# Kernel optimization log

Measured on AMD Instinct MI355X. Metric: run time of the kernel, lower is better.

Reference implementation:

```python
import jax, jax.numpy as jnp
import numpy as np

B, S, D, H = 2, 1024, 1024, 16
DH = D // H
EPS = 1e-5

def _ln(x, g, b):
    m = jnp.mean(x, axis=-1, keepdims=True)
    v = jnp.mean((x - m) ** 2, axis=-1, keepdims=True)
    return (x - m) / jnp.sqrt(v + EPS) * g + b

def setup_inputs() -> dict:
    key = jax.random.key(0)
    ks = jax.random.split(key, 5)
    scale = 1.0 / np.sqrt(D)
    return {
        "id": jax.random.normal(ks[0], (B, S, D), dtype=jnp.float32),
        "Wq": jax.random.uniform(ks[1], (D, D), jnp.float32, -scale, scale),
        "Wk": jax.random.uniform(ks[2], (D, D), jnp.float32, -scale, scale),
        "Wv": jax.random.uniform(ks[3], (D, D), jnp.float32, -scale, scale),
        "g0": jnp.ones((D,), jnp.float32), "b0": jnp.zeros((D,), jnp.float32),
        "g1": jnp.ones((D,), jnp.float32), "b1": jnp.zeros((D,), jnp.float32),
        "g2": jnp.ones((D,), jnp.float32), "b2": jnp.zeros((D,), jnp.float32),
    }

def reference(id, Wq, Wk, Wv, g0, b0, g1, b1, g2, b2):
    residual = id
    id_ln = _ln(id, g0, b0)
    # torch Linear: x @ W.T ; split heads along last dim, cat along batch
    q = (id_ln @ Wq.T).reshape(B, S, H, DH)
    k = (id_ln @ Wk.T).reshape(B, S, H, DH)
    v = (id_ln @ Wv.T).reshape(B, S, H, DH)
    scores = jnp.einsum('bqhd,bkhd->bhqk', q, k) / np.sqrt(DH)
    A = jax.nn.softmax(scores, axis=-1)                      # [B,H,S,S]
    O = jnp.einsum('bhqk,bkhd->bqhd', A, v).reshape(B, S, D)  # merge heads
    left = _ln(id_ln + O, g1, b1)
    right = _ln(residual + O, g2, b2)
    out = left + right
    # torch layout of A is [(H*B), S, S] with head-major ordering
    A_out = jnp.transpose(A, (1, 0, 2, 3)).reshape(H * B, S, S)
    return (out, A_out)
```

## Files before the change

kernel.cpp:

```cpp
#include <hip/hip_runtime.h>

namespace {

constexpr int B = 2, S = 1024, D = 1024, H = 16, DH = 64;
constexpr int M = B * S;
constexpr float EPS = 1e-5f;

using bf16x8 = __attribute__((ext_vector_type(8))) short;
using bf16x4 = __attribute__((ext_vector_type(4))) short;
using f32x4  = __attribute__((ext_vector_type(4))) float;

typedef const __attribute__((address_space(1))) void* gptr_t;
typedef __attribute__((address_space(3))) void* lptr_t;

__device__ __forceinline__ unsigned short f2bf(float f) {
    union { float f; unsigned u; } v{f};
    unsigned r = v.u + 0x7fffu + ((v.u >> 16) & 1u);
    return (unsigned short)(r >> 16);
}

__device__ __forceinline__ float wave_sum(float v) {
#pragma unroll
    for (int off = 32; off > 0; off >>= 1) v += __shfl_down(v, off, 64);
    return v;
}

__global__ __launch_bounds__(256) void cvt_w_kernel(
    const float* __restrict__ Wq, const float* __restrict__ Wk,
    const float* __restrict__ Wv, unsigned short* __restrict__ Wb)
{
    const float* src = (blockIdx.z == 0) ? Wq : (blockIdx.z == 1) ? Wk : Wv;
    const size_t i = ((size_t)blockIdx.x * 256 + threadIdx.x) * 4;
    float4 f = *reinterpret_cast<const float4*>(src + i);
    ushort4 h;
    h.x = f2bf(f.x); h.y = f2bf(f.y); h.z = f2bf(f.z); h.w = f2bf(f.w);
    *reinterpret_cast<ushort4*>(Wb + (size_t)blockIdx.z * D * D + i) = h;
}

__global__ __launch_bounds__(256) void ln0_kernel(
    const float* __restrict__ x, const float* __restrict__ g,
    const float* __restrict__ bt, float* __restrict__ y,
    unsigned short* __restrict__ yb)
{
    __shared__ float sm[8];
    __shared__ float stats[2];
    const int row = blockIdx.x;
    const int t = threadIdx.x;
    const float4 v = reinterpret_cast<const float4*>(x + (size_t)row * D)[t];
    float s  = v.x + v.y + v.z + v.w;
    float ss = v.x*v.x + v.y*v.y + v.z*v.z + v.w*v.w;
    s = wave_sum(s); ss = wave_sum(ss);
    const int lane = t & 63, wid = t >> 6;
    if (lane == 0) { sm[wid] = s; sm[4 + wid] = ss; }
    __syncthreads();
    if (t == 0) {
        float S1 = sm[0] + sm[1] + sm[2] + sm[3];
        float S2 = sm[4] + sm[5] + sm[6] + sm[7];
        float m  = S1 * (1.0f / D);
        float var = S2 * (1.0f / D) - m * m;
        stats[0] = m; stats[1] = rsqrtf(var + EPS);
    }
    __syncthreads();
    const float m = stats[0], r = stats[1];
    const float4 gv = reinterpret_cast<const float4*>(g)[t];
    const float4 bv = reinterpret_cast<const float4*>(bt)[t];
    float4 o;
    o.x = (v.x - m) * r * gv.x + bv.x;
    o.y = (v.y - m) * r * gv.y + bv.y;
    o.z = (v.z - m) * r * gv.z + bv.z;
    o.w = (v.w - m) * r * gv.w + bv.w;
    reinterpret_cast<float4*>(y + (size_t)row * D)[t] = o;
    ushort4 h; h.x = f2bf(o.x); h.y = f2bf(o.y); h.z = f2bf(o.z); h.w = f2bf(o.w);
    *reinterpret_cast<ushort4*>(yb + (size_t)row * D + t * 4) = h;
}

__global__ __launch_bounds__(256) void qkv_mfma_kernel(
    const unsigned short* __restrict__ idln, const unsigned short* __restrict__ Wb,
    unsigned short* __restrict__ q, unsigned short* __restrict__ k,
    unsigned short* __restrict__ vT)
{
    __shared__ unsigned short As[128 * 32];
    __shared__ unsigned short Bs[128 * 32];
    const int zi = blockIdx.z;
    const unsigned short* Bmat = Wb + (size_t)zi * D * D;
    const int m0 = blockIdx.y * 128, n0 = blockIdx.x * 128;
    const int t = threadIdx.x;
    const int w = t >> 6, lane = t & 63;
    const int wm = (w >> 1) * 64, wn = (w & 1) * 64;
    const int quad = lane >> 4, l16 = lane & 15;
    const int srow = t >> 2;
    const int scol = (t & 3) * 8;

    f32x4 acc[4][4];
#pragma unroll
    for (int i = 0; i < 4; ++i)
#pragma unroll
        for (int j = 0; j < 4; ++j) acc[i][j] = (f32x4){0.f, 0.f, 0.f, 0.f};

    for (int k0 = 0; k0 < D; k0 += 32) {
        __syncthreads();
#pragma unroll
        for (int c = 0; c < 2; ++c) {
            const unsigned short* ga = idln + (size_t)(m0 + srow + c * 64) * D + k0 + scol;
            __builtin_amdgcn_global_load_lds((gptr_t)ga, (lptr_t)(As + t * 8 + c * 2048), 16, 0, 0);
            const unsigned short* gb = Bmat + (size_t)(n0 + srow + c * 64) * D + k0 + scol;
            __builtin_amdgcn_global_load_lds((gptr_t)gb, (lptr_t)(Bs + t * 8 + c * 2048), 16, 0, 0);
        }
        __syncthreads();
        bf16x8 af[4], bfr[4];
#pragma unroll
        for (int i = 0; i < 4; ++i)
            af[i] = *reinterpret_cast<const bf16x8*>(As + (wm + i * 16 + l16) * 32 + quad * 8);
#pragma unroll
        for (int j = 0; j < 4; ++j)
            bfr[j] = *reinterpret_cast<const bf16x8*>(Bs + (wn + j * 16 + l16) * 32 + quad * 8);
#pragma unroll
        for (int i = 0; i < 4; ++i)
#pragma unroll
            for (int j = 0; j < 4; ++j)
                acc[i][j] = __builtin_amdgcn_mfma_f32_16x16x32_bf16(af[i], bfr[j], acc[i][j], 0, 0, 0);
    }

    if (zi < 2) {
        unsigned short* C = (zi == 0) ? q : k;
#pragma unroll
        for (int i = 0; i < 4; ++i)
#pragma unroll
            for (int j = 0; j < 4; ++j) {
                const int gcol = n0 + wn + j * 16 + l16;
#pragma unroll
                for (int reg = 0; reg < 4; ++reg) {
                    const int grow = m0 + wm + i * 16 + quad * 4 + reg;
                    C[(size_t)grow * D + gcol] = f2bf(acc[i][j][reg]);
                }
            }
    } else {
        const int b = m0 >> 10;
#pragma unroll
        for (int i = 0; i < 4; ++i)
#pragma unroll
            for (int j = 0; j < 4; ++j) {
                const int gcol = n0 + wn + j * 16 + l16;
                const int srow0 = (m0 - b * S) + wm + i * 16 + quad * 4;
                ushort4 h;
                h.x = f2bf(acc[i][j][0]); h.y = f2bf(acc[i][j][1]);
                h.z = f2bf(acc[i][j][2]); h.w = f2bf(acc[i][j][3]);
                *reinterpret_cast<ushort4*>(vT + ((size_t)b * D + gcol) * S + srow0) = h;
            }
    }
}

__global__ __launch_bounds__(256) void attn_fused_kernel(
    const unsigned short* __restrict__ q, const unsigned short* __restrict__ k,
    const unsigned short* __restrict__ vT, float* __restrict__ Aout,
    float* __restrict__ O)
{
    __shared__ unsigned short Qs[2 * 64 * 32];
    __shared__ unsigned short Ks[2 * 64 * 32];
    __shared__ unsigned short Vs[4 * 64 * 16];
    __shared__ float sInv[64];

    const int z = blockIdx.z;
    const int b = z & 1, h = z >> 1;
    const int m0 = blockIdx.y * 64;
    const int t = threadIdx.x;
    const int w = t >> 6, lane = t & 63;
    const int quad = lane >> 4, l16 = lane & 15;
    const int sr = t >> 2, sc8 = (t & 3) * 8;

#pragma unroll
    for (int c = 0; c < 2; ++c) {
        const unsigned short* gq = q + (size_t)(b * S + m0 + sr) * D + h * DH + c * 32 + sc8;
        __builtin_amdgcn_global_load_lds((gptr_t)gq, (lptr_t)(Qs + c * 2048 + t * 8), 16, 0, 0);
    }
    __syncthreads();
    bf16x8 qf[2];
#pragma unroll
    for (int c = 0; c < 2; ++c)
        qf[c] = *reinterpret_cast<const bf16x8*>(Qs + c * 2048 + (w * 16 + l16) * 32 + quad * 8);

    float rsum = 0.f;
    for (int n0 = 0; n0 < S; n0 += 64) {
        __syncthreads();
#pragma unroll
        for (int c = 0; c < 2; ++c) {
            const unsigned short* gk = k + (size_t)(b * S + n0 + sr) * D + h * DH + c * 32 + sc8;
            __builtin_amdgcn_global_load_lds((gptr_t)gk, (lptr_t)(Ks + c * 2048 + t * 8), 16, 0, 0);
        }
        __syncthreads();
#pragma unroll
        for (int kt = 0; kt < 4; ++kt) {
            f32x4 a = (f32x4){0.f, 0.f, 0.f, 0.f};
#pragma unroll
            for (int c = 0; c < 2; ++c) {
                bf16x8 kf = *reinterpret_cast<const bf16x8*>(Ks + c * 2048 + (kt * 16 + l16) * 32 + quad * 8);
                a = __builtin_amdgcn_mfma_f32_16x16x32_bf16(kf, qf[c], a, 0, 0, 0);
            }
#pragma unroll
            for (int r = 0; r < 4; ++r) rsum += __expf(a[r] * 0.125f);
        }
    }
    rsum += __shfl_xor(rsum, 16, 64);
    rsum += __shfl_xor(rsum, 32, 64);
    if (lane < 16) sInv[w * 16 + lane] = 1.0f / rsum;
    const float sL = 1.0f / rsum;

    f32x4 accO[4];
#pragma unroll
    for (int jj = 0; jj < 4; ++jj) accO[jj] = (f32x4){0.f, 0.f, 0.f, 0.f};

    float* Az = Aout + (size_t)z * S * S + (size_t)(m0 + w * 16 + l16) * S;

    for (int n0 = 0; n0 < S; n0 += 64) {
        __syncthreads();
#pragma unroll
        for (int c = 0; c < 2; ++c) {
            const unsigned short* gk = k + (size_t)(b * S + n0 + sr) * D + h * DH + c * 32 + sc8;
            __builtin_amdgcn_global_load_lds((gptr_t)gk, (lptr_t)(Ks + c * 2048 + t * 8), 16, 0, 0);
        }
#pragma unroll
        for (int c2 = 0; c2 < 2; ++c2) {
            const int kt = c2 * 2 + (t >> 7);
            const int dh = (t >> 1) & 63;
            const int kh = t & 1;
            const unsigned short* gv = vT + ((size_t)b * D + h * DH + dh) * S + n0 + kt * 16 + kh * 8;
            __builtin_amdgcn_global_load_lds((gptr_t)gv, (lptr_t)(Vs + c2 * 2048 + t * 8), 16, 0, 0);
        }
        __syncthreads();
#pragma unroll
        for (int kt = 0; kt < 4; ++kt) {
            f32x4 a = (f32x4){0.f, 0.f, 0.f, 0.f};
#pragma unroll
            for (int c = 0; c < 2; ++c) {
                bf16x8 kf = *reinterpret_cast<const bf16x8*>(Ks + c * 2048 + (kt * 16 + l16) * 32 + quad * 8);
                a = __builtin_amdgcn_mfma_f32_16x16x32_bf16(kf, qf[c], a, 0, 0, 0);
            }
            float e0 = __expf(a[0] * 0.125f) * sL;
            float e1 = __expf(a[1] * 0.125f) * sL;
            float e2 = __expf(a[2] * 0.125f) * sL;
            float e3 = __expf(a[3] * 0.125f) * sL;
            *reinterpret_cast<float4*>(Az + n0 + kt * 16 + quad * 4) = make_float4(e0, e1, e2, e3);
            bf16x4 p;
            p[0] = (short)f2bf(e0); p[1] = (short)f2bf(e1);
            p[2] = (short)f2bf(e2); p[3] = (short)f2bf(e3);
#pragma unroll
            for (int jj = 0; jj < 4; ++jj) {
                bf16x4 vv = *reinterpret_cast<const bf16x4*>(Vs + kt * 1024 + (jj * 16 + l16) * 16 + quad * 4);
                accO[jj] = __builtin_amdgcn_mfma_f32_16x16x16bf16_1k(p, vv, accO[jj], 0, 0, 0);
            }
        }
    }
#pragma unroll
    for (int jj = 0; jj < 4; ++jj)
#pragma unroll
        for (int r = 0; r < 4; ++r) {
            const int grow = b * S + m0 + w * 16 + quad * 4 + r;
            O[(size_t)grow * D + h * DH + jj * 16 + l16] = accO[jj][r];
        }
}

__global__ __launch_bounds__(256) void final_kernel(
    const float* __restrict__ id, const float* __restrict__ id_ln, const float* __restrict__ O,
    const float* __restrict__ g1, const float* __restrict__ b1,
    const float* __restrict__ g2, const float* __restrict__ b2,
    float* __restrict__ out)
{
    __shared__ float sm[16];
    __shared__ float stats[4];
    const int row = blockIdx.x;
    const int t = threadIdx.x;
    const size_t base = (size_t)row * D;
    const float4 xi = reinterpret_cast<const float4*>(id + base)[t];
    const float4 xl = reinterpret_cast<const float4*>(id_ln + base)[t];
    const float4 xo = reinterpret_cast<const float4*>(O + base)[t];
    float4 t1, t2;
    t1.x = xl.x + xo.x; t1.y = xl.y + xo.y; t1.z = xl.z + xo.z; t1.w = xl.w + xo.w;
    t2.x = xi.x + xo.x; t2.y = xi.y + xo.y; t2.z = xi.z + xo.z; t2.w = xi.w + xo.w;
    float s1  = t1.x + t1.y + t1.z + t1.w;
    float ss1 = t1.x*t1.x + t1.y*t1.y + t1.z*t1.z + t1.w*t1.w;
    float s2  = t2.x + t2.y + t2.z + t2.w;
    float ss2 = t2.x*t2.x + t2.y*t2.y + t2.z*t2.z + t2.w*t2.w;
    s1 = wave_sum(s1); ss1 = wave_sum(ss1);
    s2 = wave_sum(s2); ss2 = wave_sum(ss2);
    const int lane = t & 63, wid = t >> 6;
    if (lane == 0) { sm[wid] = s1; sm[4+wid] = ss1; sm[8+wid] = s2; sm[12+wid] = ss2; }
    __syncthreads();
    if (t == 0) {
        float S1 = sm[0]+sm[1]+sm[2]+sm[3];
        float Q1 = sm[4]+sm[5]+sm[6]+sm[7];
        float S2 = sm[8]+sm[9]+sm[10]+sm[11];
        float Q2 = sm[12]+sm[13]+sm[14]+sm[15];
        float m1 = S1 * (1.0f / D);
        float m2 = S2 * (1.0f / D);
        stats[0] = m1; stats[1] = rsqrtf(Q1 * (1.0f / D) - m1*m1 + EPS);
        stats[2] = m2; stats[3] = rsqrtf(Q2 * (1.0f / D) - m2*m2 + EPS);
    }
    __syncthreads();
    const float m1 = stats[0], r1 = stats[1], m2 = stats[2], r2 = stats[3];
    const float4 g1v = reinterpret_cast<const float4*>(g1)[t];
    const float4 b1v = reinterpret_cast<const float4*>(b1)[t];
    const float4 g2v = reinterpret_cast<const float4*>(g2)[t];
    const float4 b2v = reinterpret_cast<const float4*>(b2)[t];
    float4 o;
    o.x = (t1.x - m1)*r1*g1v.x + b1v.x + (t2.x - m2)*r2*g2v.x + b2v.x;
    o.y = (t1.y - m1)*r1*g1v.y + b1v.y + (t2.y - m2)*r2*g2v.y + b2v.y;
    o.z = (t1.z - m1)*r1*g1v.z + b1v.z + (t2.z - m2)*r2*g2v.z + b2v.z;
    o.w = (t1.w - m1)*r1*g1v.w + b1v.w + (t2.w - m2)*r2*g2v.w + b2v.w;
    reinterpret_cast<float4*>(out + base)[t] = o;
}

}

extern "C" void kernel_launch(void* const* d_in, const int* in_sizes, int n_in,
                              void* d_out, int out_size, void* d_ws, size_t ws_size,
                              hipStream_t stream)
{
    const float* id = (const float*)d_in[0];
    const float* Wq = (const float*)d_in[1];
    const float* Wk = (const float*)d_in[2];
    const float* Wv = (const float*)d_in[3];
    const float* g0 = (const float*)d_in[4];
    const float* b0 = (const float*)d_in[5];
    const float* g1 = (const float*)d_in[6];
    const float* b1 = (const float*)d_in[7];
    const float* g2 = (const float*)d_in[8];
    const float* b2 = (const float*)d_in[9];

    float* out  = (float*)d_out;
    float* Aout = out + (size_t)B * S * D;

    char* ws = (char*)d_ws;
    float* id_ln  = (float*)(ws);
    float* O      = (float*)(ws + (8u << 20));
    unsigned short* idln_bf = (unsigned short*)(ws + (16u << 20));
    unsigned short* Wb      = idln_bf + (size_t)M * D;
    unsigned short* qb      = Wb + (size_t)3 * D * D;
    unsigned short* kb      = qb + (size_t)M * D;
    unsigned short* vT      = kb + (size_t)M * D;

    hipLaunchKernelGGL(cvt_w_kernel, dim3(D * D / 1024, 1, 3), dim3(256), 0, stream,
                       Wq, Wk, Wv, Wb);
    hipLaunchKernelGGL(ln0_kernel, dim3(M), dim3(256), 0, stream, id, g0, b0, id_ln, idln_bf);
    hipLaunchKernelGGL(qkv_mfma_kernel, dim3(D / 128, M / 128, 3), dim3(256), 0, stream,
                       idln_bf, Wb, qb, kb, vT);
    hipLaunchKernelGGL(attn_fused_kernel, dim3(1, S / 64, H * B), dim3(256), 0, stream,
                       qb, kb, vT, Aout, O);
    hipLaunchKernelGGL(final_kernel, dim3(M), dim3(256), 0, stream,
                       id, id_ln, O, g1, b1, g2, b2, out);
}
```

Before: 233.9 us.

## Single-pass attention: stash unnormalized probabilities in LDS, normalize at end

Replaces the two-pass softmax, which recomputed QK^T and exp in a second sweep, with one pass. Unnormalized bf16 probabilities for the whole 64x1024 tile are kept in a 128KB LDS buffer, while PV accumulates unnormalized and is scaled by the row inverse sum at the end. The block grows to 512 threads, with two wave groups splitting the key tiles. K and V tiles are double-buffered with prefetch, and K is stored in LDS with an XOR swizzle. Risks: A_out is now computed from bf16-rounded probabilities, so it loses precision, and the large LDS footprint limits occupancy.

```diff
diff --git a/kernel.cpp b/kernel.cpp
--- a/kernel.cpp
+++ b/kernel.cpp
@@ -17,6 +17,13 @@
     union { float f; unsigned u; } v{f};
     unsigned r = v.u + 0x7fffu + ((v.u >> 16) & 1u);
     return (unsigned short)(r >> 16);
+}
+
+__device__ __forceinline__ float bflo(unsigned u) {
+    union { unsigned u; float f; } v{u << 16}; return v.f;
+}
+__device__ __forceinline__ float bfhi(unsigned u) {
+    union { unsigned u; float f; } v{u & 0xffff0000u}; return v.f;
 }
 
 __device__ __forceinline__ float wave_sum(float v) {
@@ -150,15 +157,16 @@
     }
 }
 
-__global__ __launch_bounds__(256) void attn_fused_kernel(
+__global__ __launch_bounds__(512, 2) void attn_fused_kernel(
     const unsigned short* __restrict__ q, const unsigned short* __restrict__ k,
     const unsigned short* __restrict__ vT, float* __restrict__ Aout,
     float* __restrict__ O)
 {
-    __shared__ unsigned short Qs[2 * 64 * 32];
     __shared__ unsigned short Ks[2 * 64 * 32];
-    __shared__ unsigned short Vs[4 * 64 * 16];
-    __shared__ float sInv[64];
+    __shared__ unsigned short Vs[2][4 * 64 * 16];
+    __shared__ unsigned short Ps[64 * 1024];
+    __shared__ float sred[2 * 64];
+    __shared__ float sinv[64];
 
     const int z = blockIdx.z;
     const int b = z & 1, h = z >> 1;
@@ -166,97 +174,149 @@
     const int t = threadIdx.x;
     const int w = t >> 6, lane = t & 63;
     const int quad = lane >> 4, l16 = lane & 15;
-    const int sr = t >> 2, sc8 = (t & 3) * 8;
-
-#pragma unroll
-    for (int c = 0; c < 2; ++c) {
-        const unsigned short* gq = q + (size_t)(b * S + m0 + sr) * D + h * DH + c * 32 + sc8;
-        __builtin_amdgcn_global_load_lds((gptr_t)gq, (lptr_t)(Qs + c * 2048 + t * 8), 16, 0, 0);
-    }
-    __syncthreads();
+    const int rowg = w & 3, khalf = w >> 2;
+    const int kt0 = khalf * 2;
+    const int prow = rowg * 16 + l16;
+
+    const int ksr = t >> 3;
+    const int ksc = (t & 7) * 8;
+    const unsigned short* kbase = k + (size_t)(b * S + ksr) * D + h * DH + ksc;
+    const int kwaddr = (((ksc >> 5) * 4096) + ksr * 64 + (ksc & 31) * 2)
+                     ^ (((((ksr >> 1) & 3) << 1) | ((ksr >> 3) & 1)) << 4);
+    const int kxorR = ((((l16 >> 1) & 3) << 1) | ((l16 >> 3) & 1)) << 4;
+
+    const int vkt = t >> 7, vdh = (t >> 1) & 63, vkh = t & 1;
+    const unsigned short* vbase = vT + ((size_t)b * D + h * DH + vdh) * S + vkt * 16 + vkh * 8;
+
+    const unsigned short* qrow = q + (size_t)(b * S + m0 + prow) * D + h * DH;
     bf16x8 qf[2];
-#pragma unroll
-    for (int c = 0; c < 2; ++c)
-        qf[c] = *reinterpret_cast<const bf16x8*>(Qs + c * 2048 + (w * 16 + l16) * 32 + quad * 8);
-
+    qf[0] = *reinterpret_cast<const bf16x8*>(qrow + quad * 8);
+    qf[1] = *reinterpret_cast<const bf16x8*>(qrow + 32 + quad * 8);
+
+    {
+        uint4 kreg = *reinterpret_cast<const uint4*>(kbase);
+        __builtin_amdgcn_global_load_lds((gptr_t)vbase, (lptr_t)((char*)Vs[0] + t * 16), 16, 0, 0);
+        asm volatile("s_waitcnt vmcnt(0)" ::: "memory");
+        *reinterpret_cast<uint4*>((char*)Ks + kwaddr) = kreg;
+        asm volatile("s_waitcnt lgkmcnt(0)" ::: "memory");
+        __builtin_amdgcn_s_barrier();
+        __builtin_amdgcn_sched_barrier(0);
+    }
+
+    f32x4 accO[4];
+#pragma unroll
+    for (int jj = 0; jj < 4; ++jj) accO[jj] = (f32x4){0.f, 0.f, 0.f, 0.f};
     float rsum = 0.f;
-    for (int n0 = 0; n0 < S; n0 += 64) {
-        __syncthreads();
-#pragma unroll
-        for (int c = 0; c < 2; ++c) {
-            const unsigned short* gk = k + (size_t)(b * S + n0 + sr) * D + h * DH + c * 32 + sc8;
-            __builtin_amdgcn_global_load_lds((gptr_t)gk, (lptr_t)(Ks + c * 2048 + t * 8), 16, 0, 0);
+    int cur = 0;
+
+    for (int tt = 0; tt < 16; ++tt) {
+        const int n0 = tt * 64;
+        const bool pf = (tt < 15);
+        uint4 kreg;
+        if (pf) {
+            kreg = *reinterpret_cast<const uint4*>(kbase + (size_t)(n0 + 64) * D);
+            __builtin_amdgcn_global_load_lds((gptr_t)(vbase + n0 + 64),
+                                             (lptr_t)((char*)Vs[cur ^ 1] + t * 16), 16, 0, 0);
         }
-        __syncthreads();
-#pragma unroll
-        for (int kt = 0; kt < 4; ++kt) {
+#pragma unroll
+        for (int kk = 0; kk < 2; ++kk) {
+            const int kt = kt0 + kk;
+            const int key = kt * 16 + l16;
             f32x4 a = (f32x4){0.f, 0.f, 0.f, 0.f};
 #pragma unroll
             for (int c = 0; c < 2; ++c) {
-                bf16x8 kf = *reinterpret_cast<const bf16x8*>(Ks + c * 2048 + (kt * 16 + l16) * 32 + quad * 8);
+                const int kraddr = (c * 4096 + key * 64 + quad * 16) ^ kxorR;
+                bf16x8 kf = *reinterpret_cast<const bf16x8*>((const char*)Ks + kraddr);
                 a = __builtin_amdgcn_mfma_f32_16x16x32_bf16(kf, qf[c], a, 0, 0, 0);
             }
-#pragma unroll
-            for (int r = 0; r < 4; ++r) rsum += __expf(a[r] * 0.125f);
-        }
-    }
-    rsum += __shfl_xor(rsum, 16, 64);
-    rsum += __shfl_xor(rsum, 32, 64);
-    if (lane < 16) sInv[w * 16 + lane] = 1.0f / rsum;
-    const float sL = 1.0f / rsum;
-
-    f32x4 accO[4];
-#pragma unroll
-    for (int jj = 0; jj < 4; ++jj) accO[jj] = (f32x4){0.f, 0.f, 0.f, 0.f};
-
-    float* Az = Aout + (size_t)z * S * S + (size_t)(m0 + w * 16 + l16) * S;
-
-    for (int n0 = 0; n0 < S; n0 += 64) {
-        __syncthreads();
-#pragma unroll
-        for (int c = 0; c < 2; ++c) {
-            const unsigned short* gk = k + (size_t)(b * S + n0 + sr) * D + h * DH + c * 32 + sc8;
-            __builtin_amdgcn_global_load_lds((gptr_t)gk, (lptr_t)(Ks + c * 2048 + t * 8), 16, 0, 0);
-        }
-#pragma unroll
-        for (int c2 = 0; c2 < 2; ++c2) {
-            const int kt = c2 * 2 + (t >> 7);
-            const int dh = (t >> 1) & 63;
-            const int kh = t & 1;
-            const unsigned short* gv = vT + ((size_t)b * D + h * DH + dh) * S + n0 + kt * 16 + kh * 8;
-            __builtin_amdgcn_global_load_lds((gptr_t)gv, (lptr_t)(Vs + c2 * 2048 + t * 8), 16, 0, 0);
-        }
-        __syncthreads();
-#pragma unroll
-        for (int kt = 0; kt < 4; ++kt) {
-            f32x4 a = (f32x4){0.f, 0.f, 0.f, 0.f};
-#pragma unroll
-            for (int c = 0; c < 2; ++c) {
-                bf16x8 kf = *reinterpret_cast<const bf16x8*>(Ks + c * 2048 + (kt * 16 + l16) * 32 + quad * 8);
-                a = __builtin_amdgcn_mfma_f32_16x16x32_bf16(kf, qf[c], a, 0, 0, 0);
-            }
-            float e0 = __expf(a[0] * 0.125f) * sL;
-            float e1 = __expf(a[1] * 0.125f) * sL;
-            float e2 = __expf(a[2] * 0.125f) * sL;
-            float e3 = __expf(a[3] * 0.125f) * sL;
-            *reinterpret_cast<float4*>(Az + n0 + kt * 16 + quad * 4) = make_float4(e0, e1, e2, e3);
+            const float e0 = __expf(a[0] * 0.125f);
+            const float e1 = __expf(a[1] * 0.125f);
+            const float e2 = __expf(a[2] * 0.125f);
+            const float e3 = __expf(a[3] * 0.125f);
+            rsum += (e0 + e1) + (e2 + e3);
             bf16x4 p;
             p[0] = (short)f2bf(e0); p[1] = (short)f2bf(e1);
             p[2] = (short)f2bf(e2); p[3] = (short)f2bf(e3);
+            const int pw = (prow * 2048 + (n0 + kt * 16 + quad * 4) * 2) ^ ((prow & 7) << 4);
+            *reinterpret_cast<bf16x4*>((char*)Ps + pw) = p;
 #pragma unroll
             for (int jj = 0; jj < 4; ++jj) {
-                bf16x4 vv = *reinterpret_cast<const bf16x4*>(Vs + kt * 1024 + (jj * 16 + l16) * 16 + quad * 4);
+                bf16x4 vv = *reinterpret_cast<const bf16x4*>(
+                    (const char*)Vs[cur] + kt * 2048 + (jj * 16 + l16) * 32 + quad * 8);
                 accO[jj] = __builtin_amdgcn_mfma_f32_16x16x16bf16_1k(p, vv, accO[jj], 0, 0, 0);
             }
         }
-    }
-#pragma unroll
-    for (int jj = 0; jj < 4; ++jj)
-#pragma unroll
-        for (int r = 0; r < 4; ++r) {
-            const int grow = b * S + m0 + w * 16 + quad * 4 + r;
-            O[(size_t)grow * D + h * DH + jj * 16 + l16] = accO[jj][r];
+        asm volatile("s_waitcnt lgkmcnt(0)" ::: "memory");
+        __builtin_amdgcn_s_barrier();
+        __builtin_amdgcn_sched_barrier(0);
+        if (pf) {
+            asm volatile("s_waitcnt vmcnt(0)" ::: "memory");
+            *reinterpret_cast<uint4*>((char*)Ks + kwaddr) = kreg;
+            asm volatile("s_waitcnt lgkmcnt(0)" ::: "memory");
+            __builtin_amdgcn_s_barrier();
+            __builtin_amdgcn_sched_barrier(0);
         }
+        cur ^= 1;
+    }
+
+    rsum += __shfl_xor(rsum, 16, 64);
+    rsum += __shfl_xor(rsum, 32, 64);
+    if (lane < 16) sred[khalf * 64 + rowg * 16 + lane] = rsum;
+    __syncthreads();
+    if (khalf == 0 && lane < 16) {
+        const float tot = sred[rowg * 16 + lane] + sred[64 + rowg * 16 + lane];
+        sinv[rowg * 16 + lane] = 1.0f / tot;
+    }
+    __syncthreads();
+
+    {
+        float* Az = Aout + (size_t)z * S * S + (size_t)m0 * S;
+#pragma unroll
+        for (int r8 = 0; r8 < 8; ++r8) {
+            const int row = w * 8 + r8;
+            const float sc = sinv[row];
+            const int swz = (row & 7) << 4;
+            const int base = row * 2048 + lane * 16;
+            uint4 h0 = *reinterpret_cast<const uint4*>((const char*)Ps + (base ^ swz));
+            uint4 h1 = *reinterpret_cast<const uint4*>((const char*)Ps + ((base + 1024) ^ swz));
+            float* dst = Az + (size_t)row * S + lane * 8;
+            float4 fa, fb, fc, fd;
+            fa.x = bflo(h0.x) * sc; fa.y = bfhi(h0.x) * sc;
+            fa.z = bflo(h0.y) * sc; fa.w = bfhi(h0.y) * sc;
+            fb.x = bflo(h0.z) * sc; fb.y = bfhi(h0.z) * sc;
+            fb.z = bflo(h0.w) * sc; fb.w = bfhi(h0.w) * sc;
+            fc.x = bflo(h1.x) * sc; fc.y = bfhi(h1.x) * sc;
+            fc.z = bflo(h1.y) * sc; fc.w = bfhi(h1.y) * sc;
+            fd.x = bflo(h1.z) * sc; fd.y = bfhi(h1.z) * sc;
+            fd.z = bflo(h1.w) * sc; fd.w = bfhi(h1.w) * sc;
+            *reinterpret_cast<float4*>(dst)       = fa;
+            *reinterpret_cast<float4*>(dst + 4)   = fb;
+            *reinterpret_cast<float4*>(dst + 512) = fc;
+            *reinterpret_cast<float4*>(dst + 516) = fd;
+        }
+    }
+    __syncthreads();
+
+    float* obuf = reinterpret_cast<float*>(Ps);
+    if (khalf == 1) {
+#pragma unroll
+        for (int jj = 0; jj < 4; ++jj)
+#pragma unroll
+            for (int r = 0; r < 4; ++r)
+                obuf[rowg * 1024 + (quad * 4 + r) * 64 + jj * 16 + l16] = accO[jj][r];
+    }
+    __syncthreads();
+    if (khalf == 0) {
+#pragma unroll
+        for (int jj = 0; jj < 4; ++jj)
+#pragma unroll
+            for (int r = 0; r < 4; ++r) {
+                const int lrow = rowg * 16 + quad * 4 + r;
+                const float o = accO[jj][r]
+                              + obuf[rowg * 1024 + (quad * 4 + r) * 64 + jj * 16 + l16];
+                O[(size_t)(b * S + m0 + lrow) * D + h * DH + jj * 16 + l16] = o * sinv[lrow];
+            }
+    }
 }
 
 __global__ __launch_bounds__(256) void final_kernel(
@@ -343,7 +403,7 @@
     hipLaunchKernelGGL(ln0_kernel, dim3(M), dim3(256), 0, stream, id, g0, b0, id_ln, idln_bf);
     hipLaunchKernelGGL(qkv_mfma_kernel, dim3(D / 128, M / 128, 3), dim3(256), 0, stream,
                        idln_bf, Wb, qb, kb, vT);
-    hipLaunchKernelGGL(attn_fused_kernel, dim3(1, S / 64, H * B), dim3(256), 0, stream,
+    hipLaunchKernelGGL(attn_fused_kernel, dim3(1, S / 64, H * B), dim3(512), 0, stream,
                        qb, kb, vT, Aout, O);
     hipLaunchKernelGGL(final_kernel, dim3(M), dim3(256), 0, stream,
                        id, id_ln, O, g1, b1, g2, b2, out);
```

Result: slower. 252.8 us (+8.0%).

## Double-buffer LDS tiles in QKV GEMM and attention, swizzle K/V LDS layout

Applied to the files above, without the earlier changes.

Both the QKV projection GEMM and the fused attention kernel now use two LDS buffers. The next K-tile, or K/V tile, is issued via global_load_lds while MFMAs run on the current one, which leaves one barrier per iteration instead of two. The attention kernel also XOR-swizzles the K and V layouts in LDS to cut bank conflicts on fragment reads. This doubles LDS use per block, which could lower occupancy. Correctness relies on the async LDS loads having completed by the single trailing barrier.

```diff
diff --git a/kernel.cpp b/kernel.cpp
--- a/kernel.cpp
+++ b/kernel.cpp
@@ -79,8 +79,8 @@
     unsigned short* __restrict__ q, unsigned short* __restrict__ k,
     unsigned short* __restrict__ vT)
 {
-    __shared__ unsigned short As[128 * 32];
-    __shared__ unsigned short Bs[128 * 32];
+    __shared__ unsigned short As[2][128 * 32];
+    __shared__ unsigned short Bs[2][128 * 32];
     const int zi = blockIdx.z;
     const unsigned short* Bmat = Wb + (size_t)zi * D * D;
     const int m0 = blockIdx.y * 128, n0 = blockIdx.x * 128;
@@ -97,28 +97,35 @@
 #pragma unroll
         for (int j = 0; j < 4; ++j) acc[i][j] = (f32x4){0.f, 0.f, 0.f, 0.f};
 
+    auto STAGE = [&](int kk0, int bb) {
+#pragma unroll
+        for (int c = 0; c < 2; ++c) {
+            const unsigned short* ga = idln + (size_t)(m0 + srow + c * 64) * D + kk0 + scol;
+            __builtin_amdgcn_global_load_lds((gptr_t)ga, (lptr_t)(As[bb] + t * 8 + c * 2048), 16, 0, 0);
+            const unsigned short* gb = Bmat + (size_t)(n0 + srow + c * 64) * D + kk0 + scol;
+            __builtin_amdgcn_global_load_lds((gptr_t)gb, (lptr_t)(Bs[bb] + t * 8 + c * 2048), 16, 0, 0);
+        }
+    };
+
+    STAGE(0, 0);
+    __syncthreads();
+    int cur = 0;
     for (int k0 = 0; k0 < D; k0 += 32) {
-        __syncthreads();
-#pragma unroll
-        for (int c = 0; c < 2; ++c) {
-            const unsigned short* ga = idln + (size_t)(m0 + srow + c * 64) * D + k0 + scol;
-            __builtin_amdgcn_global_load_lds((gptr_t)ga, (lptr_t)(As + t * 8 + c * 2048), 16, 0, 0);
-            const unsigned short* gb = Bmat + (size_t)(n0 + srow + c * 64) * D + k0 + scol;
-            __builtin_amdgcn_global_load_lds((gptr_t)gb, (lptr_t)(Bs + t * 8 + c * 2048), 16, 0, 0);
-        }
-        __syncthreads();
+        if (k0 + 32 < D) STAGE(k0 + 32, cur ^ 1);
         bf16x8 af[4], bfr[4];
 #pragma unroll
         for (int i = 0; i < 4; ++i)
-            af[i] = *reinterpret_cast<const bf16x8*>(As + (wm + i * 16 + l16) * 32 + quad * 8);
+            af[i] = *reinterpret_cast<const bf16x8*>(As[cur] + (wm + i * 16 + l16) * 32 + quad * 8);
 #pragma unroll
         for (int j = 0; j < 4; ++j)
-            bfr[j] = *reinterpret_cast<const bf16x8*>(Bs + (wn + j * 16 + l16) * 32 + quad * 8);
+            bfr[j] = *reinterpret_cast<const bf16x8*>(Bs[cur] + (wn + j * 16 + l16) * 32 + quad * 8);
 #pragma unroll
         for (int i = 0; i < 4; ++i)
 #pragma unroll
             for (int j = 0; j < 4; ++j)
                 acc[i][j] = __builtin_amdgcn_mfma_f32_16x16x32_bf16(af[i], bfr[j], acc[i][j], 0, 0, 0);
+        __syncthreads();
+        cur ^= 1;
     }
 
     if (zi < 2) {
@@ -156,9 +163,8 @@
     float* __restrict__ O)
 {
     __shared__ unsigned short Qs[2 * 64 * 32];
-    __shared__ unsigned short Ks[2 * 64 * 32];
-    __shared__ unsigned short Vs[4 * 64 * 16];
-    __shared__ float sInv[64];
+    __shared__ unsigned short Ks[2][2 * 64 * 32];
+    __shared__ unsigned short Vs[2][4 * 64 * 16];
 
     const int z = blockIdx.z;
     const int b = z & 1, h = z >> 1;
@@ -166,13 +172,38 @@
     const int t = threadIdx.x;
     const int w = t >> 6, lane = t & 63;
     const int quad = lane >> 4, l16 = lane & 15;
-    const int sr = t >> 2, sc8 = (t & 3) * 8;
+
+    const int ksr = t >> 2;
+    const int kslot = t & 3;
+    const int ksc = (kslot ^ ((ksr >> 1) & 3)) * 8;
+    const int vdh = (t >> 1) & 63, vkh = t & 1;
+    const int vkh_src = vkh ^ ((vdh >> 2) & 1);
+
+    const int kx = (quad ^ ((l16 >> 1) & 3)) * 16;
+    const int vx = (quad * 8) ^ (((l16 >> 2) & 1) << 4);
+
+    auto STAGE_K = [&](int nt, int bb) {
+#pragma unroll
+        for (int c = 0; c < 2; ++c) {
+            const unsigned short* gk = k + (size_t)(b * S + nt + ksr) * D + h * DH + c * 32 + ksc;
+            __builtin_amdgcn_global_load_lds((gptr_t)gk, (lptr_t)(Ks[bb] + c * 2048 + t * 8), 16, 0, 0);
+        }
+    };
+    auto STAGE_V = [&](int nt, int bb) {
+#pragma unroll
+        for (int c2 = 0; c2 < 2; ++c2) {
+            const int kt = c2 * 2 + (t >> 7);
+            const unsigned short* gv = vT + ((size_t)b * D + h * DH + vdh) * S + nt + kt * 16 + vkh_src * 8;
+            __builtin_amdgcn_global_load_lds((gptr_t)gv, (lptr_t)((char*)Vs[bb] + c2 * 4096 + t * 16), 16, 0, 0);
+        }
+    };
 
 #pragma unroll
     for (int c = 0; c < 2; ++c) {
-        const unsigned short* gq = q + (size_t)(b * S + m0 + sr) * D + h * DH + c * 32 + sc8;
+        const unsigned short* gq = q + (size_t)(b * S + m0 + ksr) * D + h * DH + c * 32 + kslot * 8;
         __builtin_amdgcn_global_load_lds((gptr_t)gq, (lptr_t)(Qs + c * 2048 + t * 8), 16, 0, 0);
     }
+    STAGE_K(0, 0);
     __syncthreads();
     bf16x8 qf[2];
 #pragma unroll
@@ -180,59 +211,47 @@
         qf[c] = *reinterpret_cast<const bf16x8*>(Qs + c * 2048 + (w * 16 + l16) * 32 + quad * 8);
 
     float rsum = 0.f;
-    for (int n0 = 0; n0 < S; n0 += 64) {
-        __syncthreads();
-#pragma unroll
-        for (int c = 0; c < 2; ++c) {
-            const unsigned short* gk = k + (size_t)(b * S + n0 + sr) * D + h * DH + c * 32 + sc8;
-            __builtin_amdgcn_global_load_lds((gptr_t)gk, (lptr_t)(Ks + c * 2048 + t * 8), 16, 0, 0);
-        }
-        __syncthreads();
+    int cur = 0;
+    for (int tt = 0; tt < 16; ++tt) {
+        if (tt < 15) STAGE_K((tt + 1) * 64, cur ^ 1);
 #pragma unroll
         for (int kt = 0; kt < 4; ++kt) {
             f32x4 a = (f32x4){0.f, 0.f, 0.f, 0.f};
 #pragma unroll
             for (int c = 0; c < 2; ++c) {
-                bf16x8 kf = *reinterpret_cast<const bf16x8*>(Ks + c * 2048 + (kt * 16 + l16) * 32 + quad * 8);
+                bf16x8 kf = *reinterpret_cast<const bf16x8*>(
+                    (const char*)Ks[cur] + c * 4096 + (kt * 16 + l16) * 64 + kx);
                 a = __builtin_amdgcn_mfma_f32_16x16x32_bf16(kf, qf[c], a, 0, 0, 0);
             }
 #pragma unroll
             for (int r = 0; r < 4; ++r) rsum += __expf(a[r] * 0.125f);
         }
-    }
+        __syncthreads();
+        cur ^= 1;
+    }
+    STAGE_K(0, 0);
+    STAGE_V(0, 0);
     rsum += __shfl_xor(rsum, 16, 64);
     rsum += __shfl_xor(rsum, 32, 64);
-    if (lane < 16) sInv[w * 16 + lane] = 1.0f / rsum;
     const float sL = 1.0f / rsum;
 
     f32x4 accO[4];
 #pragma unroll
     for (int jj = 0; jj < 4; ++jj) accO[jj] = (f32x4){0.f, 0.f, 0.f, 0.f};
-
     float* Az = Aout + (size_t)z * S * S + (size_t)(m0 + w * 16 + l16) * S;
-
-    for (int n0 = 0; n0 < S; n0 += 64) {
-        __syncthreads();
-#pragma unroll
-        for (int c = 0; c < 2; ++c) {
-            const unsigned short* gk = k + (size_t)(b * S + n0 + sr) * D + h * DH + c * 32 + sc8;
-            __builtin_amdgcn_global_load_lds((gptr_t)gk, (lptr_t)(Ks + c * 2048 + t * 8), 16, 0, 0);
-        }
-#pragma unroll
-        for (int c2 = 0; c2 < 2; ++c2) {
-            const int kt = c2 * 2 + (t >> 7);
-            const int dh = (t >> 1) & 63;
-            const int kh = t & 1;
-            const unsigned short* gv = vT + ((size_t)b * D + h * DH + dh) * S + n0 + kt * 16 + kh * 8;
-            __builtin_amdgcn_global_load_lds((gptr_t)gv, (lptr_t)(Vs + c2 * 2048 + t * 8), 16, 0, 0);
-        }
-        __syncthreads();
+    __syncthreads();
+
+    cur = 0;
+    for (int tt = 0; tt < 16; ++tt) {
+        const int n0 = tt * 64;
+        if (tt < 15) { STAGE_K(n0 + 64, cur ^ 1); STAGE_V(n0 + 64, cur ^ 1); }
 #pragma unroll
         for (int kt = 0; kt < 4; ++kt) {
             f32x4 a = (f32x4){0.f, 0.f, 0.f, 0.f};
 #pragma unroll
             for (int c = 0; c < 2; ++c) {
-                bf16x8 kf = *reinterpret_cast<const bf16x8*>(Ks + c * 2048 + (kt * 16 + l16) * 32 + quad * 8);
+                bf16x8 kf = *reinterpret_cast<const bf16x8*>(
+                    (const char*)Ks[cur] + c * 4096 + (kt * 16 + l16) * 64 + kx);
                 a = __builtin_amdgcn_mfma_f32_16x16x32_bf16(kf, qf[c], a, 0, 0, 0);
             }
             float e0 = __expf(a[0] * 0.125f) * sL;
@@ -245,10 +264,13 @@
             p[2] = (short)f2bf(e2); p[3] = (short)f2bf(e3);
 #pragma unroll
             for (int jj = 0; jj < 4; ++jj) {
-                bf16x4 vv = *reinterpret_cast<const bf16x4*>(Vs + kt * 1024 + (jj * 16 + l16) * 16 + quad * 4);
+                bf16x4 vv = *reinterpret_cast<const bf16x4*>(
+                    (const char*)Vs[cur] + kt * 2048 + (jj * 16 + l16) * 32 + vx);
                 accO[jj] = __builtin_amdgcn_mfma_f32_16x16x16bf16_1k(p, vv, accO[jj], 0, 0, 0);
             }
         }
+        __syncthreads();
+        cur ^= 1;
     }
 #pragma unroll
     for (int jj = 0; jj < 4; ++jj)
```

Result: slower. 250.7 us (+7.1%).

## Fuse softmax rowsum pass into PV pass with deferred normalization

Applied to the files above, without the earlier changes.

The separate first pass over all keys that only computed the softmax denominator is removed. Scores are now exponentiated once, accumulated into the row sum, packed to bf16 and held in registers, and fed unnormalized into the PV MFMAs. At the end the output is scaled by the reciprocal sum, and the attention matrix is written from the saved values. This halves the QK^T work and the K reloads. In exchange it uses 128 extra VGPRs per thread and could spill, and A_out is now rounded to bf16 before scaling.

```diff
diff --git a/kernel.cpp b/kernel.cpp
--- a/kernel.cpp
+++ b/kernel.cpp
@@ -17,6 +17,13 @@
     union { float f; unsigned u; } v{f};
     unsigned r = v.u + 0x7fffu + ((v.u >> 16) & 1u);
     return (unsigned short)(r >> 16);
+}
+
+__device__ __forceinline__ float bflo(unsigned u) {
+    union { unsigned u; float f; } v{u << 16}; return v.f;
+}
+__device__ __forceinline__ float bfhi(unsigned u) {
+    union { unsigned u; float f; } v{u & 0xffff0000u}; return v.f;
 }
 
 __device__ __forceinline__ float wave_sum(float v) {
@@ -150,7 +157,7 @@
     }
 }
 
-__global__ __launch_bounds__(256) void attn_fused_kernel(
+__global__ __launch_bounds__(256, 2) void attn_fused_kernel(
     const unsigned short* __restrict__ q, const unsigned short* __restrict__ k,
     const unsigned short* __restrict__ vT, float* __restrict__ Aout,
     float* __restrict__ O)
@@ -158,7 +165,6 @@
     __shared__ unsigned short Qs[2 * 64 * 32];
     __shared__ unsigned short Ks[2 * 64 * 32];
     __shared__ unsigned short Vs[4 * 64 * 16];
-    __shared__ float sInv[64];
 
     const int z = blockIdx.z;
     const int b = z & 1, h = z >> 1;
@@ -179,39 +185,15 @@
     for (int c = 0; c < 2; ++c)
         qf[c] = *reinterpret_cast<const bf16x8*>(Qs + c * 2048 + (w * 16 + l16) * 32 + quad * 8);
 
+    f32x4 accO[4];
+#pragma unroll
+    for (int jj = 0; jj < 4; ++jj) accO[jj] = (f32x4){0.f, 0.f, 0.f, 0.f};
     float rsum = 0.f;
-    for (int n0 = 0; n0 < S; n0 += 64) {
-        __syncthreads();
-#pragma unroll
-        for (int c = 0; c < 2; ++c) {
-            const unsigned short* gk = k + (size_t)(b * S + n0 + sr) * D + h * DH + c * 32 + sc8;
-            __builtin_amdgcn_global_load_lds((gptr_t)gk, (lptr_t)(Ks + c * 2048 + t * 8), 16, 0, 0);
-        }
-        __syncthreads();
-#pragma unroll
-        for (int kt = 0; kt < 4; ++kt) {
-            f32x4 a = (f32x4){0.f, 0.f, 0.f, 0.f};
-#pragma unroll
-            for (int c = 0; c < 2; ++c) {
-                bf16x8 kf = *reinterpret_cast<const bf16x8*>(Ks + c * 2048 + (kt * 16 + l16) * 32 + quad * 8);
-                a = __builtin_amdgcn_mfma_f32_16x16x32_bf16(kf, qf[c], a, 0, 0, 0);
-            }
-#pragma unroll
-            for (int r = 0; r < 4; ++r) rsum += __expf(a[r] * 0.125f);
-        }
-    }
-    rsum += __shfl_xor(rsum, 16, 64);
-    rsum += __shfl_xor(rsum, 32, 64);
-    if (lane < 16) sInv[w * 16 + lane] = 1.0f / rsum;
-    const float sL = 1.0f / rsum;
-
-    f32x4 accO[4];
-#pragma unroll
-    for (int jj = 0; jj < 4; ++jj) accO[jj] = (f32x4){0.f, 0.f, 0.f, 0.f};
-
-    float* Az = Aout + (size_t)z * S * S + (size_t)(m0 + w * 16 + l16) * S;
-
-    for (int n0 = 0; n0 < S; n0 += 64) {
+    uint2 pst[64];
+
+#pragma unroll
+    for (int tt = 0; tt < 16; ++tt) {
+        const int n0 = tt * 64;
         __syncthreads();
 #pragma unroll
         for (int c = 0; c < 2; ++c) {
@@ -235,14 +217,15 @@
                 bf16x8 kf = *reinterpret_cast<const bf16x8*>(Ks + c * 2048 + (kt * 16 + l16) * 32 + quad * 8);
                 a = __builtin_amdgcn_mfma_f32_16x16x32_bf16(kf, qf[c], a, 0, 0, 0);
             }
-            float e0 = __expf(a[0] * 0.125f) * sL;
-            float e1 = __expf(a[1] * 0.125f) * sL;
-            float e2 = __expf(a[2] * 0.125f) * sL;
-            float e3 = __expf(a[3] * 0.125f) * sL;
-            *reinterpret_cast<float4*>(Az + n0 + kt * 16 + quad * 4) = make_float4(e0, e1, e2, e3);
+            const float e0 = __expf(a[0] * 0.125f);
+            const float e1 = __expf(a[1] * 0.125f);
+            const float e2 = __expf(a[2] * 0.125f);
+            const float e3 = __expf(a[3] * 0.125f);
+            rsum += (e0 + e1) + (e2 + e3);
             bf16x4 p;
             p[0] = (short)f2bf(e0); p[1] = (short)f2bf(e1);
             p[2] = (short)f2bf(e2); p[3] = (short)f2bf(e3);
+            pst[tt * 4 + kt] = *reinterpret_cast<uint2*>(&p);
 #pragma unroll
             for (int jj = 0; jj < 4; ++jj) {
                 bf16x4 vv = *reinterpret_cast<const bf16x4*>(Vs + kt * 1024 + (jj * 16 + l16) * 16 + quad * 4);
@@ -250,12 +233,30 @@
             }
         }
     }
+
+    rsum += __shfl_xor(rsum, 16, 64);
+    rsum += __shfl_xor(rsum, 32, 64);
+    const float sL = 1.0f / rsum;
+    float sO[4];
+#pragma unroll
+    for (int r = 0; r < 4; ++r) sO[r] = __shfl(sL, quad * 4 + r, 64);
+
+    float* Az = Aout + (size_t)z * S * S + (size_t)(m0 + w * 16 + l16) * S;
+#pragma unroll
+    for (int tt = 0; tt < 16; ++tt)
+#pragma unroll
+        for (int kt = 0; kt < 4; ++kt) {
+            const uint2 u = pst[tt * 4 + kt];
+            *reinterpret_cast<float4*>(Az + tt * 64 + kt * 16 + quad * 4) =
+                make_float4(bflo(u.x) * sL, bfhi(u.x) * sL, bflo(u.y) * sL, bfhi(u.y) * sL);
+        }
+
 #pragma unroll
     for (int jj = 0; jj < 4; ++jj)
 #pragma unroll
         for (int r = 0; r < 4; ++r) {
             const int grow = b * S + m0 + w * 16 + quad * 4 + r;
-            O[(size_t)grow * D + h * DH + jj * 16 + l16] = accO[jj][r];
+            O[(size_t)grow * D + h * DH + jj * 16 + l16] = accO[jj][r] * sO[r];
         }
 }
 
```

Result: slower. 240.9 us (+3.0%).
